# Performance work log

Measured on AMD Instinct MI355X. Metric: run time of the kernel, lower is better.

## Reference

```python
import jax, jax.numpy as jnp
import numpy as np

DIM = 2048
HID = 5632  # multiple_of*ceil((2/3*8192)/256)
CONV = 4
SEQ = 8192


def setup_inputs() -> dict:
    key = jax.random.key(0)
    ks = jax.random.split(key, 6)
    x = jax.random.normal(ks[0], (1, SEQ, DIM), dtype=jnp.float32)
    cu_seqlens = jnp.array([0, 2048, 4096, 6144, 8192], dtype=jnp.int32)
    s = DIM ** -0.5
    w_w = jax.random.normal(ks[1], (HID, DIM), dtype=jnp.float32) * s
    wz_w = jax.random.normal(ks[2], (HID, DIM), dtype=jnp.float32) * s
    wh_w = jax.random.normal(ks[3], (HID, DIM), dtype=jnp.float32) * s
    wo_w = jax.random.normal(ks[4], (DIM, HID), dtype=jnp.float32) * (HID ** -0.5)
    conv_w = jax.random.normal(ks[5], (HID, CONV), dtype=jnp.float32) * (CONV ** -0.5)
    return {"x": x, "cu_seqlens": cu_seqlens, "w_w": w_w, "wz_w": wz_w,
            "wh_w": wh_w, "wo_w": wo_w, "conv_w": conv_w}


def _segment_ids(cu_seqlens, seq_len):
    start = jnp.zeros((seq_len,), dtype=jnp.int32).at[cu_seqlens[:-1]].set(1)
    return start, jnp.cumsum(start)  # start marker, segment id per position


def _causal_conv(z, conv_w, seg_id):
    # z: (b, s, H); depthwise causal conv, w[:, -1] multiplies current step,
    # masked so taps never cross cu_seqlens boundaries.
    s = z.shape[1]
    out = z * conv_w[:, CONV - 1][None, None, :]
    for k in range(1, CONV):
        zs = jnp.pad(z, ((0, 0), (k, 0), (0, 0)))[:, :s]
        sid = jnp.pad(seg_id, (k, 0))[:s]
        valid = (sid == seg_id) & (jnp.arange(s) >= k)
        out = out + zs * conv_w[:, CONV - 1 - k][None, None, :] * valid[None, :, None].astype(z.dtype)
    return out


def _linear_scan(a, b):
    # h_t = a_t * h_{t-1} + b_t along axis=1, via parallel associative scan
    def combine(l, r):
        al, bl = l
        ar, br = r
        return ar * al, ar * bl + br
    _, h = jax.lax.associative_scan(combine, (a, b), axis=1)
    return h


def reference(x, cu_seqlens, w_w, wz_w, wh_w, wo_w, conv_w):
    bsz, seq_len, _ = x.shape
    w0 = jnp.einsum('bsd,hd->bsh', x, w_w)
    z = jnp.einsum('bsd,hd->bsh', x, wz_w)
    tilde_h = jnp.einsum('bsd,hd->bsh', x, wh_w)
    start, seg_id = _segment_ids(cu_seqlens, seq_len)
    z = jax.nn.sigmoid(_causal_conv(z, conv_w, seg_id))
    a = (1.0 - z) * (1 - start)[None, :, None].astype(z.dtype)  # reset state at seq starts
    b = z * tilde_h
    h = _linear_scan(a, b)
    h = h * jax.nn.silu(w0)
    return jnp.einsum('bsh,dh->bsd', h, wo_w)
```

## Files before the change

kernel.cpp:

```cpp
#include <hip/hip_runtime.h>
#include <stdint.h>

#define DIM 2048
#define HID 5632
#define SEQ 8192
#define NW3 (3*HID)
#define CONV 4
#define CHUNK 64
#define KSPLIT 4
#define KSLICE (HID/KSPLIT)

typedef __attribute__((ext_vector_type(8))) __bf16 bf16x8;
typedef __attribute__((ext_vector_type(4))) float f32x4;

__device__ __forceinline__ uint16_t f2bf(float f) {
  union { float f; uint32_t u; } v; v.f = f;
  return (uint16_t)((v.u + 0x7FFFu + ((v.u >> 16) & 1u)) >> 16);
}
__device__ __forceinline__ float bf2f(uint16_t h) {
  union { uint32_t u; float f; } v; v.u = ((uint32_t)h) << 16;
  return v.f;
}

__global__ void cvt4_kernel(const float* __restrict__ src, uint16_t* __restrict__ dst, int n4) {
  int i = blockIdx.x * blockDim.x + threadIdx.x;
  if (i >= n4) return;
  float4 v = ((const float4*)src)[i];
  ushort4 o;
  o.x = f2bf(v.x); o.y = f2bf(v.y); o.z = f2bf(v.z); o.w = f2bf(v.w);
  ((ushort4*)dst)[i] = o;
}

__device__ __forceinline__ void load_lds16(const void* g, void* l) {
  __builtin_amdgcn_global_load_lds(
      (__attribute__((address_space(1))) void*)g,
      (__attribute__((address_space(3))) void*)l, 16, 0, 0);
}

template<int LDA, int LDB, int LDC, int KLEN, int OUT_MODE, bool SWAPXY>
__global__ __launch_bounds__(256)
void gemm_bt(const uint16_t* __restrict__ A, const uint16_t* __restrict__ B,
             void* __restrict__ C)
{
  __shared__ uint16_t As[128*32];
  __shared__ uint16_t Bs[128*32];
  const int tid  = threadIdx.x;
  const int wave = tid >> 6;
  const int lane = tid & 63;
  const int row0 = (SWAPXY ? blockIdx.y : blockIdx.x) * 128;
  const int col0 = (SWAPXY ? blockIdx.x : blockIdx.y) * 128;
  const int koff = blockIdx.z * KLEN;
  const int wm = (wave & 1) * 64;
  const int wn = (wave >> 1) * 64;

  f32x4 acc[4][4];
  #pragma unroll
  for (int i=0;i<4;i++)
    #pragma unroll
    for (int j=0;j<4;j++) acc[i][j] = (f32x4){0.f,0.f,0.f,0.f};

  const int mA0 = wave*32 + (lane >> 2);
  const int kkl = (lane & 3) * 8;
  const int kq  = (lane >> 4) * 8;
  const int rm  = lane & 15;

  const uint16_t* Ab = A + (size_t)koff;
  const uint16_t* Bb = B + (size_t)koff;

  for (int k0 = 0; k0 < KLEN; k0 += 32) {
    __syncthreads();
    #pragma unroll
    for (int q = 0; q < 2; ++q) {
      int m = mA0 + q*16;
      load_lds16(Ab + (size_t)(row0 + m)*LDA + k0 + kkl, &As[(size_t)(wave*2+q)*512]);
      load_lds16(Bb + (size_t)(col0 + m)*LDB + k0 + kkl, &Bs[(size_t)(wave*2+q)*512]);
    }
    __syncthreads();
    bf16x8 af[4], bfr[4];
    #pragma unroll
    for (int i=0;i<4;i++) {
      af[i]  = *(const bf16x8*)&As[(wm + i*16 + rm)*32 + kq];
      bfr[i] = *(const bf16x8*)&Bs[(wn + i*16 + rm)*32 + kq];
    }
    #pragma unroll
    for (int i=0;i<4;i++)
      #pragma unroll
      for (int j=0;j<4;j++)
        acc[i][j] = __builtin_amdgcn_mfma_f32_16x16x32_bf16(af[i], bfr[j], acc[i][j], 0, 0, 0);
  }

  const int cr = (lane >> 4) * 4;
  const int cc = lane & 15;
  #pragma unroll
  for (int i=0;i<4;i++)
    #pragma unroll
    for (int j=0;j<4;j++) {
      int rb = row0 + wm + i*16 + cr;
      int c  = col0 + wn + j*16 + cc;
      #pragma unroll
      for (int r=0;r<4;r++) {
        float v = acc[i][j][r];
        size_t idx = (size_t)(rb+r)*LDC + c;
        if (OUT_MODE == 1)      ((uint16_t*)C)[idx] = f2bf(v);
        else if (OUT_MODE == 2) atomicAdd((float*)C + idx, v);
        else                    ((float*)C)[idx] = v;
      }
    }
}


__device__ __forceinline__ void seg_info(const int* cuv, int ns, int t, int& ss, bool& st) {
  ss = 0; st = false;
  for (int i=0;i<ns;i++) { int cv = cuv[i]; if (cv<=t && cv>ss) ss=cv; if (cv==t) st=true; }
}

__global__ void scan_chunk(const uint16_t* __restrict__ G, int qstart,
                           const uint16_t* __restrict__ zprev,
                           const float* __restrict__ convw,
                           const int* __restrict__ cu, int ncu,
                           float* __restrict__ Ach, float* __restrict__ Bch)
{
  int h = blockIdx.x * blockDim.x + threadIdx.x;
  int c = blockIdx.y;
  if (h >= HID) return;
  const uint16_t* Z  = G + HID;
  const uint16_t* TH = G + 2*HID;
  float w0c = convw[h*4+0], w1c = convw[h*4+1], w2c = convw[h*4+2], w3c = convw[h*4+3];
  int cuv[8];
  int ns = ncu - 1; if (ns > 8) ns = 8;
  for (int i=0;i<ns;i++) cuv[i] = cu[i];
  int r0 = c * CHUNK;
  int t0 = qstart + r0;
  float z1, z2, z3;
  if (c == 0) {
    z1 = (t0-1 >= 0) ? bf2f(zprev[2*HID + h]) : 0.f;
    z2 = (t0-2 >= 0) ? bf2f(zprev[1*HID + h]) : 0.f;
    z3 = (t0-3 >= 0) ? bf2f(zprev[0*HID + h]) : 0.f;
  } else {
    z1 = bf2f(Z[(size_t)(r0-1)*NW3 + h]);
    z2 = bf2f(Z[(size_t)(r0-2)*NW3 + h]);
    z3 = bf2f(Z[(size_t)(r0-3)*NW3 + h]);
  }
  float Aacc = 1.f, Bacc = 0.f;
  for (int r = r0; r < r0 + CHUNK; ++r) {
    int t = qstart + r;
    float z0 = bf2f(Z[(size_t)r*NW3 + h]);
    float th = bf2f(TH[(size_t)r*NW3 + h]);
    int ss; bool st;
    seg_info(cuv, ns, t, ss, st);
    float s = z0*w3c;
    if (t-1 >= ss) s += z1*w2c;
    if (t-2 >= ss) s += z2*w1c;
    if (t-3 >= ss) s += z3*w0c;
    float zc = 1.f/(1.f + __expf(-s));
    float a = st ? 0.f : (1.f - zc);
    float b = zc * th;
    Aacc *= a;
    Bacc = a*Bacc + b;
    z3 = z2; z2 = z1; z1 = z0;
  }
  Ach[(size_t)c*HID + h] = Aacc;
  Bch[(size_t)c*HID + h] = Bacc;
}

__global__ void scan_combine(float* __restrict__ Ach, const float* __restrict__ Bch,
                             float* __restrict__ Sc, int first, int nchunk)
{
  int h = blockIdx.x * blockDim.x + threadIdx.x;
  if (h >= HID) return;
  float s = first ? 0.f : Sc[h];
  for (int c = 0; c < nchunk; ++c) {
    size_t idx = (size_t)c*HID + h;
    float a = Ach[idx], b = Bch[idx];
    Ach[idx] = s;
    s = a*s + b;
  }
  Sc[h] = s;
}

__global__ void scan_final(uint16_t* __restrict__ G, int qstart,
                           const uint16_t* __restrict__ zprev,
                           const float* __restrict__ convw,
                           const int* __restrict__ cu, int ncu,
                           const float* __restrict__ Hin)
{
  int h = blockIdx.x * blockDim.x + threadIdx.x;
  int c = blockIdx.y;
  if (h >= HID) return;
  const uint16_t* W0 = G;
  const uint16_t* Z  = G + HID;
  uint16_t*       TH = G + 2*HID;
  float w0c = convw[h*4+0], w1c = convw[h*4+1], w2c = convw[h*4+2], w3c = convw[h*4+3];
  int cuv[8];
  int ns = ncu - 1; if (ns > 8) ns = 8;
  for (int i=0;i<ns;i++) cuv[i] = cu[i];
  int r0 = c * CHUNK;
  int t0 = qstart + r0;
  float z1, z2, z3;
  if (c == 0) {
    z1 = (t0-1 >= 0) ? bf2f(zprev[2*HID + h]) : 0.f;
    z2 = (t0-2 >= 0) ? bf2f(zprev[1*HID + h]) : 0.f;
    z3 = (t0-3 >= 0) ? bf2f(zprev[0*HID + h]) : 0.f;
  } else {
    z1 = bf2f(Z[(size_t)(r0-1)*NW3 + h]);
    z2 = bf2f(Z[(size_t)(r0-2)*NW3 + h]);
    z3 = bf2f(Z[(size_t)(r0-3)*NW3 + h]);
  }
  float state = Hin[(size_t)c*HID + h];
  for (int r = r0; r < r0 + CHUNK; ++r) {
    int t = qstart + r;
    float z0 = bf2f(Z[(size_t)r*NW3 + h]);
    float th = bf2f(TH[(size_t)r*NW3 + h]);
    int ss; bool st;
    seg_info(cuv, ns, t, ss, st);
    float s = z0*w3c;
    if (t-1 >= ss) s += z1*w2c;
    if (t-2 >= ss) s += z2*w1c;
    if (t-3 >= ss) s += z3*w0c;
    float zc = 1.f/(1.f + __expf(-s));
    float a = st ? 0.f : (1.f - zc);
    float b = zc * th;
    state = a*state + b;
    float w0v = bf2f(W0[(size_t)r*NW3 + h]);
    float silu = w0v / (1.f + __expf(-w0v));
    TH[(size_t)r*NW3 + h] = f2bf(state * silu);
    z3 = z2; z2 = z1; z1 = z0;
  }
}

__global__ void save_ztail(const uint16_t* __restrict__ G, uint16_t* __restrict__ zprev, int qrows) {
  int i = blockIdx.x * blockDim.x + threadIdx.x;
  if (i >= 3*HID) return;
  int j = i / HID;
  int h = i - j*HID;
  zprev[i] = G[(size_t)(qrows-3+j)*NW3 + HID + h];
}

extern "C" void kernel_launch(void* const* d_in, const int* in_sizes, int n_in,
                              void* d_out, int out_size, void* d_ws, size_t ws_size,
                              hipStream_t stream) {
  const float* x     = (const float*)d_in[0];
  const int*   cu    = (const int*)d_in[1];
  const float* w_w   = (const float*)d_in[2];
  const float* wz_w  = (const float*)d_in[3];
  const float* wh_w  = (const float*)d_in[4];
  const float* wo_w  = (const float*)d_in[5];
  const float* wo    = (const float*)d_in[5];
  const float* convw = (const float*)d_in[6];
  const int ncu = in_sizes[1];
  float* out = (float*)d_out;
  (void)wo;

  const size_t base = 92331008ull;
  int qrows = 2048;
  if (ws_size >= base + 8192ull*38592ull) qrows = 8192;
  else if (ws_size >= base + 4096ull*38592ull) qrows = 4096;
  const int nq = SEQ / qrows;
  const int nchunk = qrows / CHUNK;

  char* p = (char*)d_ws;
  uint16_t* w3b  = (uint16_t*)p; p += (size_t)NW3*DIM*2;
  uint16_t* wob  = (uint16_t*)p; p += (size_t)DIM*HID*2;
  float*    Sc   = (float*)p;    p += (size_t)HID*4;
  uint16_t* zprev= (uint16_t*)p; p += (size_t)3*HID*2;
  uint16_t* xseg = (uint16_t*)p; p += (size_t)qrows*DIM*2;
  uint16_t* G    = (uint16_t*)p; p += (size_t)qrows*NW3*2;
  float*    Ach  = (float*)p;    p += (size_t)nchunk*HID*4;
  float*    Bch  = (float*)p;    p += (size_t)nchunk*HID*4;

  {
    int n4 = HID*DIM/4;
    cvt4_kernel<<<(n4+255)/256, 256, 0, stream>>>(w_w,  w3b, n4);
    cvt4_kernel<<<(n4+255)/256, 256, 0, stream>>>(wz_w, w3b + (size_t)HID*DIM, n4);
    cvt4_kernel<<<(n4+255)/256, 256, 0, stream>>>(wh_w, w3b + (size_t)2*HID*DIM, n4);
    n4 = DIM*HID/4;
    cvt4_kernel<<<(n4+255)/256, 256, 0, stream>>>(wo_w, wob, n4);
  }

  if (qrows == 2048)
    hipMemsetAsync(out, 0, (size_t)out_size * sizeof(float), stream);

  for (int s = 0; s < nq; ++s) {
    const int qstart = s * qrows;

    int n4 = qrows*DIM/4;
    cvt4_kernel<<<(n4+255)/256, 256, 0, stream>>>(x + (size_t)qstart*DIM, xseg, n4);

    gemm_bt<DIM, DIM, NW3, DIM, 1, false><<<dim3(qrows/128, NW3/128), 256, 0, stream>>>(
        xseg, w3b, G);

    scan_chunk  <<<dim3(HID/256, nchunk), 256, 0, stream>>>(G, qstart, zprev, convw, cu, ncu, Ach, Bch);
    scan_combine<<<HID/256, 256, 0, stream>>>(Ach, Bch, Sc, s == 0 ? 1 : 0, nchunk);
    scan_final  <<<dim3(HID/256, nchunk), 256, 0, stream>>>(G, qstart, zprev, convw, cu, ncu, Ach);

    if (s + 1 < nq)
      save_ztail<<<(3*HID+255)/256, 256, 0, stream>>>(G, zprev, qrows);

    if (qrows == 2048) {
      gemm_bt<NW3, HID, DIM, KSLICE, 2, true><<<dim3(DIM/128, qrows/128, KSPLIT), 256, 0, stream>>>(
          G + 2*HID, wob, out + (size_t)qstart*DIM);
    } else {
      gemm_bt<NW3, HID, DIM, HID, 0, true><<<dim3(DIM/128, qrows/128), 256, 0, stream>>>(
          G + 2*HID, wob, out + (size_t)qstart*DIM);
    }
  }
}
```

Measured before the change: 1.601 ms.

## Replace 128x128 GEMM with double-buffered 256x256 tile kernel and XCD swizzle

Replaces the single-buffered 128x128 bf16 GEMM with a 512-thread 256x256 tile kernel. The new kernel uses double-buffered LDS with direct global-to-LDS loads interleaved between MFMA phases, an XOR swizzle on the K offsets to avoid LDS bank conflicts, priority raising around the MFMA blocks, and a block-index swizzle that groups neighbouring tiles per XCD. It aims to hide load latency, raise data reuse per tile and improve L2 locality in both projection GEMMs. The split-K atomic path is also extended to the 4096-row case. The larger tiles mean fewer workgroups and higher register and LDS pressure.

```diff
diff --git a/kernel.cpp b/kernel.cpp
--- a/kernel.cpp
+++ b/kernel.cpp
@@ -7,8 +7,6 @@
 #define NW3 (3*HID)
 #define CONV 4
 #define CHUNK 64
-#define KSPLIT 4
-#define KSLICE (HID/KSPLIT)
 
 typedef __attribute__((ext_vector_type(8))) __bf16 bf16x8;
 typedef __attribute__((ext_vector_type(4))) float f32x4;
@@ -37,70 +35,161 @@
       (__attribute__((address_space(3))) void*)l, 16, 0, 0);
 }
 
-template<int LDA, int LDB, int LDC, int KLEN, int OUT_MODE, bool SWAPXY>
-__global__ __launch_bounds__(256)
-void gemm_bt(const uint16_t* __restrict__ A, const uint16_t* __restrict__ B,
-             void* __restrict__ C)
+template<int LDA, int LDB, int LDC, int KLEN, int OUT_MODE>
+__global__ __launch_bounds__(512, 2)
+void gemm256(const uint16_t* __restrict__ A, const uint16_t* __restrict__ B,
+             void* __restrict__ C, int nbx)
 {
-  __shared__ uint16_t As[128*32];
-  __shared__ uint16_t Bs[128*32];
+  __shared__ alignas(16) uint16_t As[2][2][256][32];
+  __shared__ alignas(16) uint16_t Bs[2][2][256][32];
+  constexpr int NT = KLEN / 64;
+
   const int tid  = threadIdx.x;
   const int wave = tid >> 6;
   const int lane = tid & 63;
-  const int row0 = (SWAPXY ? blockIdx.y : blockIdx.x) * 128;
-  const int col0 = (SWAPXY ? blockIdx.x : blockIdx.y) * 128;
-  const int koff = blockIdx.z * KLEN;
-  const int wm = (wave & 1) * 64;
-  const int wn = (wave >> 1) * 64;
-
-  f32x4 acc[4][4];
+
+  const int nwg = (int)gridDim.x;
+  const int bid = (int)blockIdx.x;
+  const int qq  = nwg >> 3, rr = nwg & 7;
+  const int xcd = bid & 7, loc = bid >> 3;
+  const int swz = (xcd < rr ? xcd*(qq+1) : rr*(qq+1) + (xcd-rr)*qq) + loc;
+  const int row0 = (swz % nbx) * 256;
+  const int col0 = (swz / nbx) * 256;
+
+  const uint16_t* Ab = A + (size_t)blockIdx.y * KLEN;
+  const uint16_t* Bb = B + (size_t)blockIdx.y * KLEN;
+
+  const int wr = wave >> 2;
+  const int wc = wave & 3;
+  const int rm = lane & 15;
+  const int kq8 = ((lane >> 4) ^ ((rm >> 1) & 3)) * 8;
+  const int ri = wr*128 + rm;
+  const int ci = wc*64 + rm;
+
+  size_t offA0, offA1, offB0, offB1;
+  {
+    const int g0 = tid,       r0_ = g0 >> 2, k0_ = (g0 & 3) ^ ((r0_ >> 1) & 3);
+    const int g1 = 512 + tid, r1_ = g1 >> 2, k1_ = (g1 & 3) ^ ((r1_ >> 1) & 3);
+    offA0 = (size_t)(row0 + r0_)*LDA + k0_*8;
+    offA1 = (size_t)(row0 + r1_)*LDA + k1_*8;
+    offB0 = (size_t)(col0 + r0_)*LDB + k0_*8;
+    offB1 = (size_t)(col0 + r1_)*LDB + k1_*8;
+  }
+
+#define STAGE_A(kt,h,buf) do {                                              \
+    const size_t ko_ = (size_t)(kt)*64 + (size_t)(h)*32;                    \
+    load_lds16(Ab + offA0 + ko_, &As[(buf)][(h)][wave*16][0]);              \
+    load_lds16(Ab + offA1 + ko_, &As[(buf)][(h)][128 + wave*16][0]);        \
+  } while (0)
+#define STAGE_B(kt,h,buf) do {                                              \
+    const size_t ko_ = (size_t)(kt)*64 + (size_t)(h)*32;                    \
+    load_lds16(Bb + offB0 + ko_, &Bs[(buf)][(h)][wave*16][0]);              \
+    load_lds16(Bb + offB1 + ko_, &Bs[(buf)][(h)][128 + wave*16][0]);        \
+  } while (0)
+
+  f32x4 acc[8][4];
   #pragma unroll
-  for (int i=0;i<4;i++)
-    #pragma unroll
-    for (int j=0;j<4;j++) acc[i][j] = (f32x4){0.f,0.f,0.f,0.f};
-
-  const int mA0 = wave*32 + (lane >> 2);
-  const int kkl = (lane & 3) * 8;
-  const int kq  = (lane >> 4) * 8;
-  const int rm  = lane & 15;
-
-  const uint16_t* Ab = A + (size_t)koff;
-  const uint16_t* Bb = B + (size_t)koff;
-
-  for (int k0 = 0; k0 < KLEN; k0 += 32) {
-    __syncthreads();
-    #pragma unroll
-    for (int q = 0; q < 2; ++q) {
-      int m = mA0 + q*16;
-      load_lds16(Ab + (size_t)(row0 + m)*LDA + k0 + kkl, &As[(size_t)(wave*2+q)*512]);
-      load_lds16(Bb + (size_t)(col0 + m)*LDB + k0 + kkl, &Bs[(size_t)(wave*2+q)*512]);
-    }
-    __syncthreads();
+  for (int i = 0; i < 8; ++i)
+    #pragma unroll
+    for (int j = 0; j < 4; ++j) acc[i][j] = (f32x4){0.f,0.f,0.f,0.f};
+
+  STAGE_A(0,0,0); STAGE_B(0,0,0);
+  STAGE_A(0,1,0); STAGE_B(0,1,0);
+  {
+    const int t1 = (NT > 1) ? 1 : 0;
+    STAGE_A(t1,0,1); STAGE_B(t1,0,1);
+  }
+  asm volatile("s_waitcnt vmcnt(8)" ::: "memory");
+  __builtin_amdgcn_s_barrier();
+
+  #pragma unroll 1
+  for (int t = 0; t < NT; ++t) {
+    const int c   = t & 1;
+    const int tn1 = (t+1 < NT) ? t+1 : NT-1;
+    const int tn2 = (t+2 < NT) ? t+2 : NT-1;
     bf16x8 af[4], bfr[4];
-    #pragma unroll
-    for (int i=0;i<4;i++) {
-      af[i]  = *(const bf16x8*)&As[(wm + i*16 + rm)*32 + kq];
-      bfr[i] = *(const bf16x8*)&Bs[(wn + i*16 + rm)*32 + kq];
-    }
-    #pragma unroll
-    for (int i=0;i<4;i++)
+
+    #pragma unroll
+    for (int i = 0; i < 4; ++i) af[i]  = *(const bf16x8*)&As[c][0][ri + i*16][kq8];
+    #pragma unroll
+    for (int j = 0; j < 4; ++j) bfr[j] = *(const bf16x8*)&Bs[c][0][ci + j*16][kq8];
+    STAGE_A(tn1, 1, c^1);
+    __builtin_amdgcn_s_barrier();
+    asm volatile("s_waitcnt lgkmcnt(0)" ::: "memory");
+    __builtin_amdgcn_sched_barrier(0);
+    __builtin_amdgcn_s_setprio(1);
+    #pragma unroll
+    for (int i = 0; i < 4; ++i)
       #pragma unroll
-      for (int j=0;j<4;j++)
+      for (int j = 0; j < 4; ++j)
         acc[i][j] = __builtin_amdgcn_mfma_f32_16x16x32_bf16(af[i], bfr[j], acc[i][j], 0, 0, 0);
-  }
+    __builtin_amdgcn_s_setprio(0);
+    __builtin_amdgcn_s_barrier();
+
+    #pragma unroll
+    for (int i = 0; i < 4; ++i) af[i] = *(const bf16x8*)&As[c][0][ri + (i+4)*16][kq8];
+    STAGE_B(tn1, 1, c^1);
+    __builtin_amdgcn_s_barrier();
+    asm volatile("s_waitcnt lgkmcnt(0)" ::: "memory");
+    __builtin_amdgcn_sched_barrier(0);
+    __builtin_amdgcn_s_setprio(1);
+    #pragma unroll
+    for (int i = 0; i < 4; ++i)
+      #pragma unroll
+      for (int j = 0; j < 4; ++j)
+        acc[i+4][j] = __builtin_amdgcn_mfma_f32_16x16x32_bf16(af[i], bfr[j], acc[i+4][j], 0, 0, 0);
+    __builtin_amdgcn_s_setprio(0);
+    asm volatile("s_waitcnt vmcnt(8)" ::: "memory");
+    __builtin_amdgcn_s_barrier();
+
+    #pragma unroll
+    for (int i = 0; i < 4; ++i) af[i]  = *(const bf16x8*)&As[c][1][ri + i*16][kq8];
+    #pragma unroll
+    for (int j = 0; j < 4; ++j) bfr[j] = *(const bf16x8*)&Bs[c][1][ci + j*16][kq8];
+    STAGE_A(tn2, 0, c);
+    __builtin_amdgcn_s_barrier();
+    asm volatile("s_waitcnt lgkmcnt(0)" ::: "memory");
+    __builtin_amdgcn_sched_barrier(0);
+    __builtin_amdgcn_s_setprio(1);
+    #pragma unroll
+    for (int i = 0; i < 4; ++i)
+      #pragma unroll
+      for (int j = 0; j < 4; ++j)
+        acc[i][j] = __builtin_amdgcn_mfma_f32_16x16x32_bf16(af[i], bfr[j], acc[i][j], 0, 0, 0);
+    __builtin_amdgcn_s_setprio(0);
+    __builtin_amdgcn_s_barrier();
+
+    #pragma unroll
+    for (int i = 0; i < 4; ++i) af[i] = *(const bf16x8*)&As[c][1][ri + (i+4)*16][kq8];
+    STAGE_B(tn2, 0, c);
+    __builtin_amdgcn_s_barrier();
+    asm volatile("s_waitcnt lgkmcnt(0)" ::: "memory");
+    __builtin_amdgcn_sched_barrier(0);
+    __builtin_amdgcn_s_setprio(1);
+    #pragma unroll
+    for (int i = 0; i < 4; ++i)
+      #pragma unroll
+      for (int j = 0; j < 4; ++j)
+        acc[i+4][j] = __builtin_amdgcn_mfma_f32_16x16x32_bf16(af[i], bfr[j], acc[i+4][j], 0, 0, 0);
+    __builtin_amdgcn_s_setprio(0);
+    asm volatile("s_waitcnt vmcnt(8)" ::: "memory");
+    __builtin_amdgcn_s_barrier();
+  }
+#undef STAGE_A
+#undef STAGE_B
 
   const int cr = (lane >> 4) * 4;
   const int cc = lane & 15;
   #pragma unroll
-  for (int i=0;i<4;i++)
-    #pragma unroll
-    for (int j=0;j<4;j++) {
-      int rb = row0 + wm + i*16 + cr;
-      int c  = col0 + wn + j*16 + cc;
+  for (int i = 0; i < 8; ++i)
+    #pragma unroll
+    for (int j = 0; j < 4; ++j) {
+      const int r_ = row0 + wr*128 + i*16 + cr;
+      const int c_ = col0 + wc*64  + j*16 + cc;
       #pragma unroll
-      for (int r=0;r<4;r++) {
-        float v = acc[i][j][r];
-        size_t idx = (size_t)(rb+r)*LDC + c;
+      for (int r = 0; r < 4; ++r) {
+        const float v = acc[i][j][r];
+        const size_t idx = (size_t)(r_ + r)*LDC + c_;
         if (OUT_MODE == 1)      ((uint16_t*)C)[idx] = f2bf(v);
         else if (OUT_MODE == 2) atomicAdd((float*)C + idx, v);
         else                    ((float*)C)[idx] = v;
@@ -245,11 +334,9 @@
   const float* wz_w  = (const float*)d_in[3];
   const float* wh_w  = (const float*)d_in[4];
   const float* wo_w  = (const float*)d_in[5];
-  const float* wo    = (const float*)d_in[5];
   const float* convw = (const float*)d_in[6];
   const int ncu = in_sizes[1];
   float* out = (float*)d_out;
-  (void)wo;
 
   const size_t base = 92331008ull;
   int qrows = 2048;
@@ -277,7 +364,7 @@
     cvt4_kernel<<<(n4+255)/256, 256, 0, stream>>>(wo_w, wob, n4);
   }
 
-  if (qrows == 2048)
+  if (qrows < 8192)
     hipMemsetAsync(out, 0, (size_t)out_size * sizeof(float), stream);
 
   for (int s = 0; s < nq; ++s) {
@@ -286,8 +373,11 @@
     int n4 = qrows*DIM/4;
     cvt4_kernel<<<(n4+255)/256, 256, 0, stream>>>(x + (size_t)qstart*DIM, xseg, n4);
 
-    gemm_bt<DIM, DIM, NW3, DIM, 1, false><<<dim3(qrows/128, NW3/128), 256, 0, stream>>>(
-        xseg, w3b, G);
+    {
+      const int nbx = qrows / 256;
+      gemm256<DIM, DIM, NW3, DIM, 1><<<dim3(nbx * (NW3/256), 1), 512, 0, stream>>>(
+          xseg, w3b, G, nbx);
+    }
 
     scan_chunk  <<<dim3(HID/256, nchunk), 256, 0, stream>>>(G, qstart, zprev, convw, cu, ncu, Ach, Bch);
     scan_combine<<<HID/256, 256, 0, stream>>>(Ach, Bch, Sc, s == 0 ? 1 : 0, nchunk);
@@ -296,12 +386,15 @@
     if (s + 1 < nq)
       save_ztail<<<(3*HID+255)/256, 256, 0, stream>>>(G, zprev, qrows);
 
-    if (qrows == 2048) {
-      gemm_bt<NW3, HID, DIM, KSLICE, 2, true><<<dim3(DIM/128, qrows/128, KSPLIT), 256, 0, stream>>>(
-          G + 2*HID, wob, out + (size_t)qstart*DIM);
+    if (qrows == 8192) {
+      gemm256<NW3, HID, DIM, HID, 0><<<dim3(32*(DIM/256), 1), 512, 0, stream>>>(
+          G + 2*HID, wob, out + (size_t)qstart*DIM, 32);
+    } else if (qrows == 4096) {
+      gemm256<NW3, HID, DIM, HID/2, 2><<<dim3(16*(DIM/256), 2), 512, 0, stream>>>(
+          G + 2*HID, wob, out + (size_t)qstart*DIM, 16);
     } else {
-      gemm_bt<NW3, HID, DIM, HID, 0, true><<<dim3(DIM/128, qrows/128), 256, 0, stream>>>(
-          G + 2*HID, wob, out + (size_t)qstart*DIM);
+      gemm256<NW3, HID, DIM, HID/4, 2><<<dim3(8*(DIM/256), 4), 512, 0, stream>>>(
+          G + 2*HID, wob, out + (size_t)qstart*DIM, 8);
     }
   }
 }
```

Result: slower. 1.659 ms (+3.6%).
